# Kernel optimization log

Hardware: AMD Instinct MI355X
Metric: run time of the kernel (lower is better)

## Reference

```python
import jax, jax.numpy as jnp
import numpy as np

HIDDEN = 2048
N_HEADS = 16
N_KV_HEADS = 4
HEAD_DIM = HIDDEN // N_HEADS  # 128
ROPE_THETA = 10000.0


def setup_inputs() -> dict:
    key = jax.random.key(0)
    ks = jax.random.split(key, 5)
    B, S = 2, 2048
    scale = 0.02
    return {
        "hidden_states": jax.random.normal(ks[0], (B, S, HIDDEN), jnp.float32),
        "Wq": jax.random.normal(ks[1], (HIDDEN, N_HEADS * HEAD_DIM), jnp.float32) * scale,
        "Wk": jax.random.normal(ks[2], (HIDDEN, N_KV_HEADS * HEAD_DIM), jnp.float32) * scale,
        "Wv": jax.random.normal(ks[3], (HIDDEN, N_KV_HEADS * HEAD_DIM), jnp.float32) * scale,
        "Wo": jax.random.normal(ks[4], (HIDDEN, HIDDEN), jnp.float32) * scale,
    }


def _rope_tables(seq_len, dim, dtype):
    inv_freq = 1.0 / (ROPE_THETA ** (jnp.arange(0, dim, 2, dtype=jnp.float32) / dim))
    t = jnp.arange(seq_len, dtype=jnp.float32)
    freqs = jnp.outer(t, inv_freq)            # [S, dim/2]
    emb = jnp.concatenate([freqs, freqs], -1)  # [S, dim]
    return jnp.cos(emb).astype(dtype), jnp.sin(emb).astype(dtype)


def _rotate_half(x):
    d = x.shape[-1] // 2
    return jnp.concatenate([-x[..., d:], x[..., :d]], axis=-1)


def _mqa_forward(hidden_states, Wq, Wk, Wv, Wo):
    B, S, _ = hidden_states.shape
    q = (hidden_states @ Wq).reshape(B, S, N_HEADS, HEAD_DIM).transpose(0, 2, 1, 3)      # [B,H,S,D]
    k = (hidden_states @ Wk).reshape(B, S, N_KV_HEADS, HEAD_DIM).transpose(0, 2, 1, 3)   # [B,Hkv,S,D]
    v = (hidden_states @ Wv).reshape(B, S, N_KV_HEADS, HEAD_DIM).transpose(0, 2, 1, 3)

    cos, sin = _rope_tables(S, HEAD_DIM, q.dtype)  # [S,D]
    q = q * cos + _rotate_half(q) * sin
    k = k * cos + _rotate_half(k) * sin

    # GQA: group query heads over shared KV heads instead of repeat_kv (same math)
    g = N_HEADS // N_KV_HEADS
    qg = q.reshape(B, N_KV_HEADS, g, S, HEAD_DIM)
    scale = 1.0 / np.sqrt(HEAD_DIM)
    scores = jnp.einsum("bhgqd,bhkd->bhgqk", qg, k) * scale  # [B,Hkv,g,S,S]
    causal = jnp.tril(jnp.ones((S, S), bool))
    scores = jnp.where(causal, scores, -jnp.inf)
    probs = jax.nn.softmax(scores.astype(jnp.float32), axis=-1).astype(q.dtype)
    out = jnp.einsum("bhgqk,bhkd->bhgqd", probs, v)  # [B,Hkv,g,S,D]
    out = out.reshape(B, N_HEADS, S, HEAD_DIM).transpose(0, 2, 1, 3).reshape(B, S, HIDDEN)
    return out @ Wo


def reference(hidden_states, Wq, Wk, Wv, Wo):
    return _mqa_forward(hidden_states, Wq, Wk, Wv, Wo)
```

## Files before the change

### kernel.cpp

```cpp
#include <hip/hip_runtime.h>
#include <hip/hip_bf16.h>
#include <cstdint>
#include <cstddef>

#define HIDDEN   2048
#define NH       16
#define NKV      4
#define HD       128
#define SEQ      2048
#define BATCH    2
#define NTOK     (BATCH*SEQ)
#define QKV_LD   3072
#define KOFF     2048
#define VOFF     2560
#define SM_SCALE 0.08838834764831845f
#define LOG2E    1.4426950408889634f

typedef __attribute__((ext_vector_type(8)))  short bf16x8;
typedef __attribute__((ext_vector_type(4)))  float f32x4v;
typedef __attribute__((ext_vector_type(16))) float f32x16;
typedef unsigned short ushort_t;

__device__ __forceinline__ unsigned short f2bf(float f) {
  return __builtin_bit_cast(unsigned short, __float2bfloat16(f));
}
__device__ __forceinline__ float bf2f(ushort_t u) {
  return __builtin_bit_cast(float, (unsigned)u << 16);
}
__device__ __forceinline__ unsigned pack2(float a, float b) {
  return (unsigned)f2bf(a) | ((unsigned)f2bf(b) << 16);
}

__device__ __forceinline__ void gload16(const void* g, void* l) {
  __builtin_amdgcn_global_load_lds(
      (const __attribute__((address_space(1))) unsigned int*)g,
      (__attribute__((address_space(3))) unsigned int*)l, 16, 0, 0);
}

__global__ __launch_bounds__(256) void conv_f2b(
    const float* __restrict__ in, ushort_t* __restrict__ out, int n8)
{
  const int i = blockIdx.x*256 + threadIdx.x;
  if (i >= n8) return;
  const float4 a = ((const float4*)in)[2*i];
  const float4 b = ((const float4*)in)[2*i + 1];
  uint4 r;
  r.x = pack2(a.x, a.y); r.y = pack2(a.z, a.w);
  r.z = pack2(b.x, b.y); r.w = pack2(b.z, b.w);
  ((uint4*)out)[i] = r;
}

__global__ __launch_bounds__(256) void transpose_f2b(
    const float* __restrict__ W, ushort_t* __restrict__ Wt, int K, int N)
{
  __shared__ float tile[32][33];
  const int n0 = blockIdx.x*32, k0 = blockIdx.y*32;
  const int tx = threadIdx.x & 31, ty = threadIdx.x >> 5;
  #pragma unroll
  for (int i = 0; i < 4; ++i)
    tile[ty*4 + i][tx] = W[(size_t)(k0 + ty*4 + i)*N + n0 + tx];
  __syncthreads();
  #pragma unroll
  for (int i = 0; i < 4; ++i) {
    const int nl = ty*4 + i;
    Wt[(size_t)(n0 + nl)*K + k0 + tx] = f2bf(tile[tx][nl]);
  }
}

template<int BN, bool B16OUT>
__global__ __launch_bounds__(512, 1) void bt_gemm2(
    const ushort_t* __restrict__ A, const ushort_t* __restrict__ Bt,
    void* __restrict__ Cv, int ldc)
{
  constexpr int WN = BN/64;
  constexpr int WM = 8/WN;
  constexpr int MF = 16/WM;
  constexpr int BROUNDS = BN/64;
  constexpr int BUFB = 32768 + BN*128;
  __shared__ char smem[2*BUFB];

  const int t = threadIdx.x, lane = t & 63, w = t >> 6;
  const int wm = w / WN, wn = w % WN;
  const int bm = blockIdx.y*256, bn = blockIdx.x*BN;
  const int lr = lane & 15, lg = lane >> 4;

  f32x4v acc[MF][4];
  #pragma unroll
  for (int mf = 0; mf < MF; ++mf)
    #pragma unroll
    for (int nf = 0; nf < 4; ++nf)
      #pragma unroll
      for (int r = 0; r < 4; ++r) acc[mf][nf][r] = 0.f;

  const char* Ab = (const char*)A;
  const char* Bb = (const char*)Bt;

  auto stage = [&](int kt2, int d) {
    char* ab = smem + d*BUFB;
    char* bb = ab + 32768;
    const int ktb = kt2*128;
    #pragma unroll
    for (int u = 0; u < 4; ++u) {
      const int idx = u*512 + t;
      const int row = idx >> 3;
      const int kb  = ((idx & 7)*16) ^ ((row & 7) << 4);
      gload16(Ab + (size_t)(bm + row)*4096 + ktb + kb, ab + idx*16);
    }
    #pragma unroll
    for (int u = 0; u < BROUNDS; ++u) {
      const int idx = u*512 + t;
      const int row = idx >> 3;
      const int kb  = ((idx & 7)*16) ^ ((row & 7) << 4);
      gload16(Bb + (size_t)(bn + row)*4096 + ktb + kb, bb + idx*16);
    }
  };

  stage(0, 0);
  __syncthreads();

#define PHASE(q) { \
    bf16x8 af0k0, af0k1, af1k0, af1k1; \
    { const int rm = wm*(MF*16) + (2*(q))*16 + lr; \
      const char* ap = asp + rm*128; \
      const int sw = (rm & 7) << 4; \
      af0k0 = *(const bf16x8*)(ap + ((lg*16) ^ sw)); \
      af0k1 = *(const bf16x8*)(ap + ((64 + lg*16) ^ sw)); } \
    { const int rm = wm*(MF*16) + (2*(q)+1)*16 + lr; \
      const char* ap = asp + rm*128; \
      const int sw = (rm & 7) << 4; \
      af1k0 = *(const bf16x8*)(ap + ((lg*16) ^ sw)); \
      af1k1 = *(const bf16x8*)(ap + ((64 + lg*16) ^ sw)); } \
    __builtin_amdgcn_s_setprio(1); \
    _Pragma("unroll") \
    for (int nf = 0; nf < 4; ++nf) { \
      acc[2*(q)][nf]   = __builtin_amdgcn_mfma_f32_16x16x32_bf16(af0k0, bfr[nf][0], acc[2*(q)][nf],   0,0,0); \
      acc[2*(q)][nf]   = __builtin_amdgcn_mfma_f32_16x16x32_bf16(af0k1, bfr[nf][1], acc[2*(q)][nf],   0,0,0); \
      acc[2*(q)+1][nf] = __builtin_amdgcn_mfma_f32_16x16x32_bf16(af1k0, bfr[nf][0], acc[2*(q)+1][nf], 0,0,0); \
      acc[2*(q)+1][nf] = __builtin_amdgcn_mfma_f32_16x16x32_bf16(af1k1, bfr[nf][1], acc[2*(q)+1][nf], 0,0,0); \
    } \
    __builtin_amdgcn_s_setprio(0); }

  int cur = 0;
  for (int kt = 0; kt < 32; ++kt) {
    if (kt < 31) stage(kt + 1, cur ^ 1);
    const char* asp = smem + cur*BUFB;
    const char* bsp = asp + 32768;
    bf16x8 bfr[4][2];
    #pragma unroll
    for (int nf = 0; nf < 4; ++nf) {
      const int rn = wn*64 + nf*16 + lr;
      const char* bp = bsp + rn*128;
      const int sw = (rn & 7) << 4;
      bfr[nf][0] = *(const bf16x8*)(bp + ((lg*16) ^ sw));
      bfr[nf][1] = *(const bf16x8*)(bp + ((64 + lg*16) ^ sw));
    }
    PHASE(0)
    PHASE(1)
    if constexpr (MF == 8) {
      PHASE(2)
      PHASE(3)
    }
    __syncthreads();
    cur ^= 1;
  }
#undef PHASE

  #pragma unroll
  for (int mf = 0; mf < MF; ++mf) {
    const int m = bm + wm*(MF*16) + mf*16 + lg*4;
    #pragma unroll
    for (int nf = 0; nf < 4; ++nf) {
      const int n = bn + wn*64 + nf*16 + lr;
      #pragma unroll
      for (int r = 0; r < 4; ++r) {
        if constexpr (B16OUT)
          ((ushort_t*)Cv)[(size_t)(m + r)*ldc + n] = f2bf(acc[mf][nf][r]);
        else
          ((float*)Cv)[(size_t)(m + r)*ldc + n] = acc[mf][nf][r];
      }
    }
  }
}

__global__ __launch_bounds__(256) void rope_conv(
    const ushort_t* __restrict__ QKVb, ushort_t* __restrict__ Qo,
    ushort_t* __restrict__ Ko)
{
  const int total = NTOK * (NH + NKV) * (HD/2);
  int idx = blockIdx.x * 256 + threadIdx.x;
  if (idx >= total) return;
  const int i   = idx & 63;
  int tmp = idx >> 6;
  const int hs  = tmp % (NH + NKV);
  const int tkn = tmp / (NH + NKV);
  const int s   = tkn & (SEQ - 1);
  const int b   = tkn >> 11;
  const float invf = expf(-(float)i * 0.14391156831212787f);
  float sn, cs;
  sincosf((float)s * invf, &sn, &cs);
  const size_t base = (size_t)tkn * QKV_LD + (hs < NH ? hs * HD : KOFF + (hs - NH) * HD);
  const float x0 = bf2f(QKVb[base + i]);
  const float x1 = bf2f(QKVb[base + i + 64]);
  const float y0 = x0 * cs - x1 * sn;
  const float y1 = x1 * cs + x0 * sn;
  if (hs < NH) {
    ushort_t* q = Qo + (size_t)tkn * HIDDEN + hs * HD;
    q[i]      = f2bf(y0 * (SM_SCALE * LOG2E));
    q[i + 64] = f2bf(y1 * (SM_SCALE * LOG2E));
  } else {
    ushort_t* k = Ko + ((size_t)(b*NKV + (hs - NH))*SEQ + s) * HD;
    k[i]      = f2bf(y0);
    k[i + 64] = f2bf(y1);
  }
}

__global__ __launch_bounds__(256) void vt_conv(
    const ushort_t* __restrict__ QKVb, ushort_t* __restrict__ Vtb)
{
  __shared__ ushort_t tile[32][33];
  const int s0 = blockIdx.x*32;
  const int d0 = (blockIdx.y & 3)*32;
  const int bk = blockIdx.y >> 2;
  const int b = bk >> 2, hk = bk & 3;
  const int tx = threadIdx.x & 31, ty = threadIdx.x >> 5;
  #pragma unroll
  for (int i = 0; i < 4; ++i) {
    const int sl = ty*4 + i;
    tile[sl][tx] = QKVb[(size_t)(b*SEQ + s0 + sl)*QKV_LD + VOFF + hk*HD + d0 + tx];
  }
  __syncthreads();
  #pragma unroll
  for (int i = 0; i < 4; ++i) {
    const int dl = ty*4 + i;
    Vtb[((size_t)bk*HD + d0 + dl)*SEQ + s0 + tx] = tile[tx][dl];
  }
}

__global__ __launch_bounds__(256) void attn_mfma11(
    const ushort_t* __restrict__ Qb, const ushort_t* __restrict__ Kb,
    const ushort_t* __restrict__ Vtb, ushort_t* __restrict__ O)
{
  __shared__ char smem[65536];

  const int bx = blockIdx.x;
  const int qt = 63 - (int)blockIdx.y;
  const int b = bx >> 2, hk = bx & 3;
  const int t = threadIdx.x, w = t >> 6, lane = t & 63;
  const int c = lane & 31, hi = lane >> 5;
  const int h = hk*4 + w;
  const int qw0 = qt*32;
  const int qg  = qw0 + c;
  const int nsteps = (qt + 2) >> 1;

  const char* Kbb = (const char*)(Kb + (size_t)(b*NKV + hk)*SEQ*HD);
  const char* Vbb = (const char*)(Vtb + (size_t)(b*NKV + hk)*HD*SEQ);

  int ksrc[4], vsrc[4], ldst[4];
  #pragma unroll
  for (int u = 0; u < 4; ++u) {
    const int idx = u*256 + t;
    const int krow = idx >> 4, kof = (idx & 15) << 4;
    ksrc[u] = krow*256 + (kof ^ ((krow & 15) << 4));
    const int vd = idx >> 3,  vof = (idx & 7) << 4;
    vsrc[u] = vd*(SEQ*2) + (vof ^ ((vd & 7) << 4));
    ldst[u] = idx*16;
  }

  bf16x8 qf[8];
  {
    const ushort_t* qrow = Qb + (size_t)(b*SEQ + qg)*HIDDEN + h*HD;
    #pragma unroll
    for (int kc = 0; kc < 8; ++kc)
      qf[kc] = *(const bf16x8*)(qrow + kc*16 + hi*8);
  }

  f32x16 ot[4];
  #pragma unroll
  for (int nc = 0; nc < 4; ++nc)
    #pragma unroll
    for (int r = 0; r < 16; ++r) ot[nc][r] = 0.f;
  float m = -1e30f, l = 0.f;

  #pragma unroll
  for (int u = 0; u < 4; ++u) {
    gload16(Kbb + ksrc[u], smem + ldst[u]);
    gload16(Vbb + vsrc[u], smem + 32768 + ldst[u]);
  }
  __syncthreads();

  int cur = 0;
  for (int kt = 0; kt < nsteps; ++kt) {
    if (kt + 1 < nsteps) {
      const int nb = cur ^ 1;
      const size_t kto = (size_t)(kt + 1) * 16384;
      const int    vto = (kt + 1) * 128;
      #pragma unroll
      for (int u = 0; u < 4; ++u) {
        gload16(Kbb + kto + ksrc[u], smem + nb*16384 + ldst[u]);
        gload16(Vbb + vto + vsrc[u], smem + 32768 + nb*16384 + ldst[u]);
      }
    }
    const char* klds = smem + cur*16384;
    const char* vlds = smem + 32768 + cur*16384;
    f32x16 s[2];
    #pragma unroll
    for (int kn = 0; kn < 2; ++kn)
      #pragma unroll
      for (int r = 0; r < 16; ++r) s[kn][r] = 0.f;
    #pragma unroll
    for (int kn = 0; kn < 2; ++kn) {
      const int row = kn*32 + c;
      const int sw = (row & 15) << 4;
      #pragma unroll
      for (int kc = 0; kc < 8; ++kc) {
        const bf16x8 ka = *(const bf16x8*)(klds + row*256 + ((kc*32 + hi*16) ^ sw));
        s[kn] = __builtin_amdgcn_mfma_f32_32x32x16_bf16(ka, qf[kc], s[kn], 0, 0, 0);
      }
    }
    if (kt == nsteps - 1) {
      #pragma unroll
      for (int kn = 0; kn < 2; ++kn)
        #pragma unroll
        for (int r = 0; r < 16; ++r) {
          const int kg_ = kt*64 + kn*32 + (r & 3) + 8*(r >> 2) + 4*hi;
          if (kg_ > qg) s[kn][r] = -1e30f;
        }
    }
    float mx[16];
    #pragma unroll
    for (int r = 0; r < 16; ++r) mx[r] = fmaxf(s[0][r], s[1][r]);
    #pragma unroll
    for (int st = 8; st > 0; st >>= 1)
      #pragma unroll
      for (int r = 0; r < 8; ++r)
        if (r < st) mx[r] = fmaxf(mx[r], mx[r + st]);
    const float pm = fmaxf(mx[0], __shfl_xor(mx[0], 32));
    if (!__all(pm - m <= 8.f)) {
      const float mnew = fmaxf(m, pm);
      const float corr = exp2f(m - mnew);
      m = mnew;
      l *= corr;
      #pragma unroll
      for (int nc = 0; nc < 4; ++nc) ot[nc] *= corr;
    }
    float ls = 0.f;
    #pragma unroll
    for (int kn = 0; kn < 2; ++kn)
      #pragma unroll
      for (int r = 0; r < 16; ++r) {
        const float p = exp2f(s[kn][r] - m);
        ls += p;
        s[kn][r] = p;
      }
    l += ls;
    #pragma unroll
    for (int kn = 0; kn < 2; ++kn) {
      #pragma unroll
      for (int rem = 0; rem < 2; ++rem) {
        const int base = 8*rem;
        const unsigned A0 = pack2(s[kn][base+0], s[kn][base+1]);
        const unsigned A1 = pack2(s[kn][base+2], s[kn][base+3]);
        const unsigned B0 = pack2(s[kn][base+4], s[kn][base+5]);
        const unsigned B1 = pack2(s[kn][base+6], s[kn][base+7]);
        const unsigned u  = hi ? A0 : B0;
        const unsigned v  = hi ? A1 : B1;
        const unsigned su = (unsigned)__shfl_xor((int)u, 32);
        const unsigned sv = (unsigned)__shfl_xor((int)v, 32);
        uint4 wv;
        wv.x = hi ? su : A0;
        wv.y = hi ? sv : A1;
        wv.z = hi ? B0 : su;
        wv.w = hi ? B1 : sv;
        const bf16x8 pb = __builtin_bit_cast(bf16x8, wv);
        const int kc = kn*2 + rem;
        #pragma unroll
        for (int nc = 0; nc < 4; ++nc) {
          const int dim = nc*32 + c;
          const bf16x8 va = *(const bf16x8*)(vlds + dim*128 + ((kc*32 + hi*16) ^ ((dim & 7) << 4)));
          ot[nc] = __builtin_amdgcn_mfma_f32_32x32x16_bf16(va, pb, ot[nc], 0, 0, 0);
        }
      }
    }
    __syncthreads();
    cur ^= 1;
  }

  const float lt = l + __shfl_xor(l, 32);
  const float inv = 1.f / lt;
  ushort_t* orow = O + (size_t)(b*SEQ + qg) * HIDDEN + h*HD;
  #pragma unroll
  for (int nc = 0; nc < 4; ++nc)
    #pragma unroll
    for (int r = 0; r < 16; r += 2) {
      const int dim = nc*32 + (r & 3) + 8*(r >> 2) + 4*hi;
      *(unsigned*)(orow + dim) = pack2(ot[nc][r]*inv, ot[nc][r+1]*inv);
    }
}

extern "C" void kernel_launch(void* const* d_in, const int* in_sizes, int n_in,
                              void* d_out, int out_size, void* d_ws, size_t ws_size,
                              hipStream_t stream)
{
  (void)in_sizes; (void)n_in; (void)out_size; (void)ws_size;
  const float* H  = (const float*)d_in[0];
  const float* Wq = (const float*)d_in[1];
  const float* Wk = (const float*)d_in[2];
  const float* Wv = (const float*)d_in[3];
  const float* Wo = (const float*)d_in[4];
  float* out = (float*)d_out;

  char* ws = (char*)d_ws;
  ushort_t* QKVb = (ushort_t*)ws;
  ushort_t* Hb   = (ushort_t*)(ws + 25165824);
  ushort_t* Qb   = Hb;
  ushort_t* Wt   = (ushort_t*)(ws + 41943040);
  ushort_t* Kb   = (ushort_t*)(ws + 54525952);
  ushort_t* Vtb  = (ushort_t*)(ws + 58720256);
  ushort_t* Oat  = (ushort_t*)(ws + 62914560);

  conv_f2b<<<4096, 256, 0, stream>>>(H, Hb, NTOK*HIDDEN/8);
  transpose_f2b<<<dim3(64, 64), 256, 0, stream>>>(Wq, Wt,                     2048, 2048);
  transpose_f2b<<<dim3(16, 64), 256, 0, stream>>>(Wk, Wt + (size_t)2048*2048, 2048, 512);
  transpose_f2b<<<dim3(16, 64), 256, 0, stream>>>(Wv, Wt + (size_t)2560*2048, 2048, 512);

  bt_gemm2<256, true><<<dim3(QKV_LD/256, NTOK/256), 512, 0, stream>>>(Hb, Wt, QKVb, QKV_LD);

  const int rope_total = NTOK * (NH + NKV) * (HD/2);
  rope_conv<<<(rope_total + 255)/256, 256, 0, stream>>>(QKVb, Qb, Kb);
  vt_conv<<<dim3(SEQ/32, 32), 256, 0, stream>>>(QKVb, Vtb);

  attn_mfma11<<<dim3(8, 64), 256, 0, stream>>>(Qb, Kb, Vtb, Oat);

  transpose_f2b<<<dim3(64, 64), 256, 0, stream>>>(Wo, Wt, 2048, 2048);
  bt_gemm2<128, false><<<dim3(HIDDEN/128, NTOK/256), 512, 0, stream>>>(Oat, Wt, out, HIDDEN);
}
```

Measured before the change: 211.2 us.

## Fuse Q RoPE into attention prologue and retile QKV GEMM to 192-wide blocks

Q rotary embedding and softmax prescaling now happen inside the attention kernel when Q fragments load straight from the QKV buffer. The separate RoPE kernel only handles K, so the extra pass that wrote and re-read Q in bf16 is gone. The QKV GEMM moves from 256-wide to 192-wide N tiles, giving 16x16 = 256 blocks to better fill the CUs. The trade-off is that each attention thread now computes expf and sincosf per Q element, and the new tile shape changes per-warp fragment counts.

Result: no change. 212.0 us (+0.4%).

```diff
diff --git a/kernel.cpp b/kernel.cpp
--- a/kernel.cpp
+++ b/kernel.cpp
@@ -67,14 +67,14 @@
   }
 }
 
-template<int BN, bool B16OUT>
+template<int BN, int WN, bool B16OUT>
 __global__ __launch_bounds__(512, 1) void bt_gemm2(
     const ushort_t* __restrict__ A, const ushort_t* __restrict__ Bt,
     void* __restrict__ Cv, int ldc)
 {
-  constexpr int WN = BN/64;
   constexpr int WM = 8/WN;
   constexpr int MF = 16/WM;
+  constexpr int NF = BN/WN/16;
   constexpr int BROUNDS = BN/64;
   constexpr int BUFB = 32768 + BN*128;
   __shared__ char smem[2*BUFB];
@@ -84,11 +84,11 @@
   const int bm = blockIdx.y*256, bn = blockIdx.x*BN;
   const int lr = lane & 15, lg = lane >> 4;
 
-  f32x4v acc[MF][4];
+  f32x4v acc[MF][NF];
   #pragma unroll
   for (int mf = 0; mf < MF; ++mf)
     #pragma unroll
-    for (int nf = 0; nf < 4; ++nf)
+    for (int nf = 0; nf < NF; ++nf)
       #pragma unroll
       for (int r = 0; r < 4; ++r) acc[mf][nf][r] = 0.f;
 
@@ -132,7 +132,7 @@
       af1k1 = *(const bf16x8*)(ap + ((64 + lg*16) ^ sw)); } \
     __builtin_amdgcn_s_setprio(1); \
     _Pragma("unroll") \
-    for (int nf = 0; nf < 4; ++nf) { \
+    for (int nf = 0; nf < NF; ++nf) { \
       acc[2*(q)][nf]   = __builtin_amdgcn_mfma_f32_16x16x32_bf16(af0k0, bfr[nf][0], acc[2*(q)][nf],   0,0,0); \
       acc[2*(q)][nf]   = __builtin_amdgcn_mfma_f32_16x16x32_bf16(af0k1, bfr[nf][1], acc[2*(q)][nf],   0,0,0); \
       acc[2*(q)+1][nf] = __builtin_amdgcn_mfma_f32_16x16x32_bf16(af1k0, bfr[nf][0], acc[2*(q)+1][nf], 0,0,0); \
@@ -145,10 +145,10 @@
     if (kt < 31) stage(kt + 1, cur ^ 1);
     const char* asp = smem + cur*BUFB;
     const char* bsp = asp + 32768;
-    bf16x8 bfr[4][2];
-    #pragma unroll
-    for (int nf = 0; nf < 4; ++nf) {
-      const int rn = wn*64 + nf*16 + lr;
+    bf16x8 bfr[NF][2];
+    #pragma unroll
+    for (int nf = 0; nf < NF; ++nf) {
+      const int rn = wn*(NF*16) + nf*16 + lr;
       const char* bp = bsp + rn*128;
       const int sw = (rn & 7) << 4;
       bfr[nf][0] = *(const bf16x8*)(bp + ((lg*16) ^ sw));
@@ -169,8 +169,8 @@
   for (int mf = 0; mf < MF; ++mf) {
     const int m = bm + wm*(MF*16) + mf*16 + lg*4;
     #pragma unroll
-    for (int nf = 0; nf < 4; ++nf) {
-      const int n = bn + wn*64 + nf*16 + lr;
+    for (int nf = 0; nf < NF; ++nf) {
+      const int n = bn + wn*(NF*16) + nf*16 + lr;
       #pragma unroll
       for (int r = 0; r < 4; ++r) {
         if constexpr (B16OUT)
@@ -182,36 +182,27 @@
   }
 }
 
-__global__ __launch_bounds__(256) void rope_conv(
-    const ushort_t* __restrict__ QKVb, ushort_t* __restrict__ Qo,
-    ushort_t* __restrict__ Ko)
-{
-  const int total = NTOK * (NH + NKV) * (HD/2);
+__global__ __launch_bounds__(256) void rope_k(
+    const ushort_t* __restrict__ QKVb, ushort_t* __restrict__ Ko)
+{
+  const int total = NTOK * NKV * (HD/2);
   int idx = blockIdx.x * 256 + threadIdx.x;
   if (idx >= total) return;
   const int i   = idx & 63;
   int tmp = idx >> 6;
-  const int hs  = tmp % (NH + NKV);
-  const int tkn = tmp / (NH + NKV);
+  const int hk  = tmp % NKV;
+  const int tkn = tmp / NKV;
   const int s   = tkn & (SEQ - 1);
   const int b   = tkn >> 11;
   const float invf = expf(-(float)i * 0.14391156831212787f);
   float sn, cs;
   sincosf((float)s * invf, &sn, &cs);
-  const size_t base = (size_t)tkn * QKV_LD + (hs < NH ? hs * HD : KOFF + (hs - NH) * HD);
+  const size_t base = (size_t)tkn * QKV_LD + KOFF + hk * HD;
   const float x0 = bf2f(QKVb[base + i]);
   const float x1 = bf2f(QKVb[base + i + 64]);
-  const float y0 = x0 * cs - x1 * sn;
-  const float y1 = x1 * cs + x0 * sn;
-  if (hs < NH) {
-    ushort_t* q = Qo + (size_t)tkn * HIDDEN + hs * HD;
-    q[i]      = f2bf(y0 * (SM_SCALE * LOG2E));
-    q[i + 64] = f2bf(y1 * (SM_SCALE * LOG2E));
-  } else {
-    ushort_t* k = Ko + ((size_t)(b*NKV + (hs - NH))*SEQ + s) * HD;
-    k[i]      = f2bf(y0);
-    k[i + 64] = f2bf(y1);
-  }
+  ushort_t* k = Ko + ((size_t)(b*NKV + hk)*SEQ + s) * HD;
+  k[i]      = f2bf(x0 * cs - x1 * sn);
+  k[i + 64] = f2bf(x1 * cs + x0 * sn);
 }
 
 __global__ __launch_bounds__(256) void vt_conv(
@@ -236,8 +227,8 @@
   }
 }
 
-__global__ __launch_bounds__(256) void attn_mfma11(
-    const ushort_t* __restrict__ Qb, const ushort_t* __restrict__ Kb,
+__global__ __launch_bounds__(256) void attn_mfma12(
+    const ushort_t* __restrict__ QKVb, const ushort_t* __restrict__ Kb,
     const ushort_t* __restrict__ Vtb, ushort_t* __restrict__ O)
 {
   __shared__ char smem[65536];
@@ -268,10 +259,24 @@
 
   bf16x8 qf[8];
   {
-    const ushort_t* qrow = Qb + (size_t)(b*SEQ + qg)*HIDDEN + h*HD;
+    const ushort_t* qrow = QKVb + (size_t)(b*SEQ + qg)*QKV_LD + h*HD;
+    bf16x8 qraw[8];
     #pragma unroll
     for (int kc = 0; kc < 8; ++kc)
-      qf[kc] = *(const bf16x8*)(qrow + kc*16 + hi*8);
+      qraw[kc] = *(const bf16x8*)(qrow + kc*16 + hi*8);
+    #pragma unroll
+    for (int kc = 0; kc < 4; ++kc)
+      #pragma unroll
+      for (int j = 0; j < 8; ++j) {
+        const int d = kc*16 + hi*8 + j;
+        const float invf = expf(-(float)d * 0.14391156831212787f);
+        float sn, cs;
+        sincosf((float)qg * invf, &sn, &cs);
+        const float x0 = bf2f((ushort_t)qraw[kc][j]);
+        const float x1 = bf2f((ushort_t)qraw[kc+4][j]);
+        qf[kc][j]   = (short)f2bf((x0*cs - x1*sn) * (SM_SCALE * LOG2E));
+        qf[kc+4][j] = (short)f2bf((x1*cs + x0*sn) * (SM_SCALE * LOG2E));
+      }
   }
 
   f32x16 ot[4];
@@ -412,7 +417,6 @@
   char* ws = (char*)d_ws;
   ushort_t* QKVb = (ushort_t*)ws;
   ushort_t* Hb   = (ushort_t*)(ws + 25165824);
-  ushort_t* Qb   = Hb;
   ushort_t* Wt   = (ushort_t*)(ws + 41943040);
   ushort_t* Kb   = (ushort_t*)(ws + 54525952);
   ushort_t* Vtb  = (ushort_t*)(ws + 58720256);
@@ -423,14 +427,13 @@
   transpose_f2b<<<dim3(16, 64), 256, 0, stream>>>(Wk, Wt + (size_t)2048*2048, 2048, 512);
   transpose_f2b<<<dim3(16, 64), 256, 0, stream>>>(Wv, Wt + (size_t)2560*2048, 2048, 512);
 
-  bt_gemm2<256, true><<<dim3(QKV_LD/256, NTOK/256), 512, 0, stream>>>(Hb, Wt, QKVb, QKV_LD);
-
-  const int rope_total = NTOK * (NH + NKV) * (HD/2);
-  rope_conv<<<(rope_total + 255)/256, 256, 0, stream>>>(QKVb, Qb, Kb);
+  bt_gemm2<192, 4, true><<<dim3(16, 16), 512, 0, stream>>>(Hb, Wt, QKVb, QKV_LD);
+
+  rope_k<<<(NTOK*NKV*64 + 255)/256, 256, 0, stream>>>(QKVb, Kb);
   vt_conv<<<dim3(SEQ/32, 32), 256, 0, stream>>>(QKVb, Vtb);
 
-  attn_mfma11<<<dim3(8, 64), 256, 0, stream>>>(Qb, Kb, Vtb, Oat);
+  attn_mfma12<<<dim3(8, 64), 256, 0, stream>>>(QKVb, Kb, Vtb, Oat);
 
   transpose_f2b<<<dim3(64, 64), 256, 0, stream>>>(Wo, Wt, 2048, 2048);
-  bt_gemm2<128, false><<<dim3(HIDDEN/128, NTOK/256), 512, 0, stream>>>(Oat, Wt, out, HIDDEN);
-}
+  bt_gemm2<128, 2, false><<<dim3(16, 16), 512, 0, stream>>>(Oat, Wt, out, HIDDEN);
+}
```
